# Kernel tuning notes

Hardware: AMD Instinct MI355X
Metric: run time of the kernel (lower is better)

## Reference

```python
import jax, jax.numpy as jnp
import numpy as np

B, C, H, W = 4, 256, 96, 96
FOUT = 32
HW = H * W
N = HW // 2  # inside/outside pixel counts (50/50 mask)


def setup_inputs() -> dict:
    key = jax.random.key(0)
    ks = jax.random.split(key, 6)
    f = jax.random.normal(ks[0], (B, C, H, W), dtype=jnp.float32)
    # deterministic alternating mask -> fixed N_in = N_out = HW/2 (jit-friendly)
    flat = (jnp.arange(HW) % 2).astype(jnp.float32)
    mask = jnp.broadcast_to(flat.reshape(1, 1, H, W), (B, 1, H, W))
    idx_in = jnp.nonzero(flat > 0.5, size=N)[0].astype(jnp.int32)   # mask == 1
    idx_out = jnp.nonzero(flat < 0.5, size=N)[0].astype(jnp.int32)  # mask == 0
    scale = 0.02
    Wq = jax.random.normal(ks[1], (FOUT, C), dtype=jnp.float32) * scale
    Wk = jax.random.normal(ks[2], (FOUT, C), dtype=jnp.float32) * scale
    Wv = jax.random.normal(ks[3], (C, C), dtype=jnp.float32) * scale
    bq = jnp.zeros((FOUT,), jnp.float32)
    bk = jnp.zeros((FOUT,), jnp.float32)
    bv = jnp.zeros((C,), jnp.float32)
    gamma = jax.random.uniform(ks[4], (1,), dtype=jnp.float32) + 0.25  # nonzero
    return {"f": f, "mask": mask, "idx_out": idx_out, "idx_in": idx_in,
            "Wq": Wq, "bq": bq, "Wk": Wk, "bk": bk, "Wv": Wv, "bv": bv,
            "gamma": gamma}


def reference(f, mask, idx_out, idx_in, Wq, bq, Wk, bk, Wv, bv, gamma):
    b, c, h, w = f.shape
    ff = f.reshape(b, c, h * w)              # (b, c, hw)
    f_out_pix = ff[:, :, idx_out]            # (b, c, Nout) gather outside pixels
    f_in_pix = ff[:, :, idx_in]              # (b, c, Nin)  gather inside pixels
    # 1x1 convs on gathered pixel sets == per-pixel linear projections
    q = jnp.einsum('oc,bcn->bon', Wq, f_out_pix) + bq[None, :, None]  # (b, fout, Nout)
    k = jnp.einsum('oc,bcn->bon', Wk, f_in_pix) + bk[None, :, None]   # (b, fout, Nin)
    v = jnp.einsum('dc,bcn->bdn', Wv, f_in_pix) + bv[None, :, None]   # (b, c, Nin)
    energy = jnp.einsum('boq,bok->bqk', q, k)       # (b, Nout, Nin)
    att = jax.nn.softmax(energy, axis=-1)
    r_v = jnp.einsum('bck,bqk->bcq', v, att)        # (b, c, Nout)
    ff2 = ff.at[:, :, idx_out].set(r_v)             # scatter write-back
    f_reshape = ff2.reshape(b, c, h, w)
    # NOTE: in torch, f_in aliases f's storage and is mutated by the scatter,
    # so f_in == f_reshape here. Reproduce that aliasing faithfully.
    f_out = f_reshape * (1.0 - mask) * gamma + f_reshape
    return (f_reshape, f_out)
```

## Files before the change

### kernel.cpp

```cpp
#include <hip/hip_runtime.h>
#include <math.h>

#define B_DIM    4
#define C_DIM    256
#define HW_DIM   9216
#define N_PIX    4608
#define FOUT_DIM 32
#define L2E      1.44269504f

typedef float  f32x4  __attribute__((ext_vector_type(4)));
typedef short  bf16x8 __attribute__((ext_vector_type(8)));

static __device__ __forceinline__ unsigned short f2bf(float x) {
    union { float f; unsigned int u; } v; v.f = x;
    unsigned int r = v.u + 0x7fffu + ((v.u >> 16) & 1u);
    return (unsigned short)(r >> 16);
}
static __device__ __forceinline__ float bf2f(unsigned short u) {
    union { unsigned int u; float f; } v; v.u = (unsigned int)u << 16; return v.f;
}

static __device__ __forceinline__ void gload_lds16(const unsigned short* g, unsigned short* l) {
    __builtin_amdgcn_global_load_lds(
        (const __attribute__((address_space(1))) void*)g,
        (__attribute__((address_space(3))) void*)l, 16, 0, 0);
}

__global__ __launch_bounds__(256) void gather_f(
    const float* __restrict__ f, const int* __restrict__ idx_out, const int* __restrict__ idx_in,
    unsigned short* __restrict__ Fo, unsigned short* __restrict__ Fi) {
    __shared__ float Fs[2][32][65];
    __shared__ int io[64], ii[64];
    const int t = threadIdx.x;
    const int n0 = blockIdx.x * 64, c0 = blockIdx.y * 32, b = blockIdx.z;
    if (t < 64) { io[t] = idx_out[n0 + t]; ii[t] = idx_in[n0 + t]; }
    __syncthreads();
    const float* fb = f + (size_t)b * C_DIM * HW_DIM;
    const int nn = t & 63, cg = t >> 6;
#pragma unroll
    for (int i = 0; i < 8; i++) {
        int c = cg * 8 + i;
        Fs[0][c][nn] = fb[(size_t)(c0 + c) * HW_DIM + io[nn]];
        Fs[1][c][nn] = fb[(size_t)(c0 + c) * HW_DIM + ii[nn]];
    }
    __syncthreads();
    {
        const int n = t >> 2, oc = (t & 3) * 8;
        size_t o = ((size_t)(b * N_PIX + n0 + n)) * C_DIM + c0 + oc;
        unsigned short tmp0[8], tmp1[8];
#pragma unroll
        for (int j = 0; j < 8; j++) {
            tmp0[j] = f2bf(Fs[0][oc + j][n]);
            tmp1[j] = f2bf(Fs[1][oc + j][n]);
        }
        *(uint4*)(Fo + o) = *(uint4*)tmp0;
        *(uint4*)(Fi + o) = *(uint4*)tmp1;
    }
}

#define FSP 40
__global__ __launch_bounds__(256) void prep(
    const unsigned short* __restrict__ Fo, const unsigned short* __restrict__ Fi,
    const float* __restrict__ Wq, const float* __restrict__ bq,
    const float* __restrict__ Wk, const float* __restrict__ bk,
    const float* __restrict__ Wv, const float* __restrict__ bv,
    unsigned short* __restrict__ Q, unsigned short* __restrict__ K,
    unsigned short* __restrict__ VT,
    const int* __restrict__ idx_out, const int* __restrict__ idx_in,
    int* __restrict__ inv) {
    __shared__ __align__(16) unsigned short SM[18688];
    const int bid = blockIdx.x, t = threadIdx.x;
    if (bid < 144) {
        unsigned short* Ws = SM;
        unsigned short* Fs = SM + 8448;
        const int n0 = (bid % 18) * 256, sel = (bid / 18) & 1, b = bid / 36;
        const unsigned short* FX = sel ? Fi : Fo;
        const float* W    = sel ? Wk : Wq;
        const float* bias = sel ? bk : bq;
        unsigned short* O = sel ? K : Q;
#pragma unroll
        for (int j = 0; j < 8; j++) {
            int fid = j * 256 + t, row = fid >> 6, f4 = fid & 63;
            float4 wv = *(const float4*)(W + (size_t)row * C_DIM + f4 * 4);
            uint2 pk;
            pk.x = f2bf(wv.x) | ((unsigned)f2bf(wv.y) << 16);
            pk.y = f2bf(wv.z) | ((unsigned)f2bf(wv.w) << 16);
            *(uint2*)(Ws + row * 264 + f4 * 4) = pk;
        }
        const int w = t >> 6, l = t & 63, lq = l & 15, lg = l >> 4;
        f32x4 acc[8];
#pragma unroll
        for (int i = 0; i < 8; i++) acc[i] = (f32x4){0.f, 0.f, 0.f, 0.f};
        for (int cs = 0; cs < 8; cs++) {
            __syncthreads();
#pragma unroll
            for (int j = 0; j < 4; j++) {
                int cid = j * 256 + t, row = cid >> 2, ch = cid & 3;
                *(uint4*)(Fs + row * FSP + ch * 8) =
                    *(const uint4*)(FX + ((size_t)(b * N_PIX + n0 + row)) * C_DIM + cs * 32 + ch * 8);
            }
            __syncthreads();
            bf16x8 bfr[2];
#pragma unroll
            for (int ob = 0; ob < 2; ob++)
                bfr[ob] = *(const bf16x8*)(Ws + (ob * 16 + lq) * 264 + cs * 32 + lg * 8);
#pragma unroll
            for (int ab = 0; ab < 4; ab++) {
                bf16x8 a = *(const bf16x8*)(Fs + (w * 64 + ab * 16 + lq) * FSP + lg * 8);
#pragma unroll
                for (int ob = 0; ob < 2; ob++)
                    acc[ab * 2 + ob] = __builtin_amdgcn_mfma_f32_16x16x32_bf16(a, bfr[ob], acc[ab * 2 + ob], 0, 0, 0);
            }
        }
#pragma unroll
        for (int ab = 0; ab < 4; ab++)
#pragma unroll
            for (int ob = 0; ob < 2; ob++)
#pragma unroll
                for (int r = 0; r < 4; r++) {
                    int n = n0 + w * 64 + ab * 16 + lg * 4 + r;
                    int o = ob * 16 + lq;
                    O[((size_t)(b * N_PIX + n)) * FOUT_DIM + o] = f2bf(acc[ab * 2 + ob][r] + bias[o]);
                }
    } else if (bid < 432) {
        unsigned short* Ws = SM;
        unsigned short* Fs = SM + 5120;
        const int vb = bid - 144;
        const int n0 = (vb % 36) * 128, d0 = ((vb / 36) & 1) * 128, b = vb / 72;
        const int w = t >> 6, wd = w & 1, wn = w >> 1, l = t & 63, lq = l & 15, lg = l >> 4;
        f32x4 acc[16];
#pragma unroll
        for (int i = 0; i < 16; i++) acc[i] = (f32x4){0.f, 0.f, 0.f, 0.f};
        for (int cs = 0; cs < 8; cs++) {
            __syncthreads();
#pragma unroll
            for (int j = 0; j < 4; j++) {
                int row = j * 32 + (t >> 3), f4 = t & 7;
                float4 wv = *(const float4*)(Wv + (size_t)(d0 + row) * C_DIM + cs * 32 + f4 * 4);
                uint2 pk;
                pk.x = f2bf(wv.x) | ((unsigned)f2bf(wv.y) << 16);
                pk.y = f2bf(wv.z) | ((unsigned)f2bf(wv.w) << 16);
                *(uint2*)(Ws + row * FSP + f4 * 4) = pk;
            }
#pragma unroll
            for (int j = 0; j < 2; j++) {
                int cid = j * 256 + t, row = cid >> 2, ch = cid & 3;
                *(uint4*)(Fs + row * FSP + ch * 8) =
                    *(const uint4*)(Fi + ((size_t)(b * N_PIX + n0 + row)) * C_DIM + cs * 32 + ch * 8);
            }
            __syncthreads();
            bf16x8 bfr[4];
#pragma unroll
            for (int nb = 0; nb < 4; nb++)
                bfr[nb] = *(const bf16x8*)(Fs + (wn * 64 + nb * 16 + lq) * FSP + lg * 8);
#pragma unroll
            for (int ab = 0; ab < 4; ab++) {
                bf16x8 a = *(const bf16x8*)(Ws + (wd * 64 + ab * 16 + lq) * FSP + lg * 8);
#pragma unroll
                for (int nb = 0; nb < 4; nb++)
                    acc[ab * 4 + nb] = __builtin_amdgcn_mfma_f32_16x16x32_bf16(a, bfr[nb], acc[ab * 4 + nb], 0, 0, 0);
            }
        }
#pragma unroll
        for (int ab = 0; ab < 4; ab++)
#pragma unroll
            for (int r = 0; r < 4; r++) {
                int d = d0 + wd * 64 + ab * 16 + lg * 4 + r;
                float bvv = bv[d];
#pragma unroll
                for (int nb = 0; nb < 4; nb++) {
                    int n = n0 + wn * 64 + nb * 16 + lq;
                    VT[((size_t)(b * C_DIM + d)) * N_PIX + n] = f2bf(acc[ab * 4 + nb][r] + bvv);
                }
            }
    } else {
        int i = (bid - 432) * 256 + t;
        if (i < N_PIX) {
            inv[idx_out[i]] = i;
            inv[idx_in[i]] = -1;
        }
    }
}

__global__ __launch_bounds__(256, 2) void flash_attn(
    const unsigned short* __restrict__ Q, const unsigned short* __restrict__ K,
    const unsigned short* __restrict__ VT,
    unsigned short* __restrict__ Rpart, float* __restrict__ lpart) {
    __shared__ __align__(16) unsigned short VB[256 * 64];
    __shared__ __align__(16) unsigned short PB[2][32 * 72];
    __shared__ float lred[2][2][2][16];
    const int t = threadIdx.x, w = t >> 6, l = t & 63, lq = l & 15, lg = l >> 4;
    const int qg = w & 1, dh = w >> 1;
    const int bid = blockIdx.x;
    const int bz = bid & 7, b = bz & 3, ks = bz >> 2;
    const int q0 = (bid >> 3) * 64 + qg * 32;
    const int d0 = dh * 128;
    const unsigned short* Qb = Q + (size_t)b * N_PIX * FOUT_DIM;
    const unsigned short* Kb = K + (size_t)b * N_PIX * FOUT_DIM;
    const unsigned short* Vb = VT + (size_t)b * C_DIM * N_PIX;
    unsigned short* Rp = Rpart + (size_t)ks * 4718592;
    float* lp = lpart + ks * (B_DIM * N_PIX);

    bf16x8 qfr[2];
    qfr[0] = *(const bf16x8*)(Qb + (size_t)(q0 + lq) * 32 + lg * 8);
    qfr[1] = *(const bf16x8*)(Qb + (size_t)(q0 + 16 + lq) * 32 + lg * 8);

    f32x4 acc[2][8];
#pragma unroll
    for (int qb = 0; qb < 2; qb++)
#pragma unroll
        for (int db = 0; db < 8; db++) acc[qb][db] = (f32x4){0.f, 0.f, 0.f, 0.f};
    float lsum[2] = {0.f, 0.f};

    int voff[8];
#pragma unroll
    for (int j = 0; j < 8; j++) {
        int row = (w * 8 + j) * 8 + (l >> 3);
        int ch  = (l & 7) ^ (row & 7);
        voff[j] = row * N_PIX + ch * 8;
    }
    const int kt0 = ks * 36;
    bf16x8 kpf[2];
    {
        int kg = kt0 * 64;
#pragma unroll
        for (int j = 0; j < 8; j++)
            gload_lds16(Vb + voff[j] + kg, VB + (w * 8 + j) * 512);
#pragma unroll
        for (int kb = 0; kb < 2; kb++)
            kpf[kb] = *(const bf16x8*)(Kb + (size_t)(kg + dh * 32 + kb * 16 + lq) * 32 + lg * 8);
    }

    const int swz = lq & 7;
#pragma unroll 1
    for (int it = 0; it < 36; it++) {
        {
            const f32x4 z4 = {0.f, 0.f, 0.f, 0.f};
#pragma unroll
            for (int qb = 0; qb < 2; qb++) {
                f32x4 s[2];
#pragma unroll
                for (int kb = 0; kb < 2; kb++)
                    s[kb] = __builtin_amdgcn_mfma_f32_16x16x32_bf16(kpf[kb], qfr[qb], z4, 0, 0, 0);
                float ps = 0.f;
#pragma unroll
                for (int kb = 0; kb < 2; kb++) {
                    float p0 = exp2f(s[kb][0] * L2E);
                    float p1 = exp2f(s[kb][1] * L2E);
                    float p2 = exp2f(s[kb][2] * L2E);
                    float p3 = exp2f(s[kb][3] * L2E);
                    ps += (p0 + p1) + (p2 + p3);
                    unsigned int u0 = (__float_as_uint(p0) + 0x8000u) >> 16;
                    unsigned int u1 = (__float_as_uint(p1) + 0x8000u) & 0xffff0000u;
                    unsigned int u2 = (__float_as_uint(p2) + 0x8000u) >> 16;
                    unsigned int u3 = (__float_as_uint(p3) + 0x8000u) & 0xffff0000u;
                    uint2 pk; pk.x = u0 | u1; pk.y = u2 | u3;
                    *(uint2*)(PB[qg] + (qb * 16 + lq) * 72 + dh * 32 + kb * 16 + lg * 4) = pk;
                }
                lsum[qb] += ps;
            }
        }
        __syncthreads();
        if (it + 1 < 36) {
            int kn = (kt0 + it + 1) * 64;
#pragma unroll
            for (int kb = 0; kb < 2; kb++)
                kpf[kb] = *(const bf16x8*)(Kb + (size_t)(kn + dh * 32 + kb * 16 + lq) * 32 + lg * 8);
        }
        bf16x8 af[2][2];
#pragma unroll
        for (int qb = 0; qb < 2; qb++) {
            af[qb][0] = *(const bf16x8*)(PB[qg] + (qb * 16 + lq) * 72 + lg * 8);
            af[qb][1] = *(const bf16x8*)(PB[qg] + (qb * 16 + lq) * 72 + 32 + lg * 8);
        }
#pragma unroll
        for (int db = 0; db < 8; db++) {
            int row = d0 + db * 16 + lq;
            bf16x8 b0 = *(const bf16x8*)(VB + row * 64 + (lg ^ swz) * 8);
            bf16x8 b1 = *(const bf16x8*)(VB + row * 64 + ((lg + 4) ^ swz) * 8);
#pragma unroll
            for (int qb = 0; qb < 2; qb++) {
                acc[qb][db] = __builtin_amdgcn_mfma_f32_16x16x32_bf16(af[qb][0], b0, acc[qb][db], 0, 0, 0);
                acc[qb][db] = __builtin_amdgcn_mfma_f32_16x16x32_bf16(af[qb][1], b1, acc[qb][db], 0, 0, 0);
            }
        }
        __syncthreads();
        if (it + 1 < 36) {
            int kn = (kt0 + it + 1) * 64;
#pragma unroll
            for (int j = 0; j < 8; j++)
                gload_lds16(Vb + voff[j] + kn, VB + (w * 8 + j) * 512);
        }
    }
#pragma unroll
    for (int qb = 0; qb < 2; qb++)
#pragma unroll
        for (int r = 0; r < 4; r++) {
            int q = q0 + qb * 16 + lg * 4 + r;
            unsigned short* rp = Rp + ((size_t)(b * N_PIX + q)) * C_DIM + d0;
#pragma unroll
            for (int db = 0; db < 8; db++)
                rp[db * 16 + lq] = f2bf(acc[qb][db][r]);
        }
#pragma unroll
    for (int qb = 0; qb < 2; qb++) {
        float v = lsum[qb];
        v += __shfl_xor(v, 16);
        v += __shfl_xor(v, 32);
        if (l < 16) lred[dh][qg][qb][l] = v;
    }
    __syncthreads();
    if (dh == 0 && l < 16) {
#pragma unroll
        for (int qb = 0; qb < 2; qb++)
            lp[b * N_PIX + q0 + qb * 16 + l] = lred[0][qg][qb][l] + lred[1][qg][qb][l];
    }
}

__global__ __launch_bounds__(256) void epilogue(
    const float* __restrict__ f, const float* __restrict__ mask,
    const unsigned short* __restrict__ R0, const unsigned short* __restrict__ R1,
    const float* __restrict__ l0, const float* __restrict__ l1,
    const int* __restrict__ inv, const float* __restrict__ gamma,
    float* __restrict__ out0, float* __restrict__ out1) {
    __shared__ __align__(16) unsigned short Rs0[32][264];
    __shared__ __align__(16) unsigned short Rs1[32][264];
    __shared__ int nns[32];
    __shared__ float lr[32];
    const int t = threadIdx.x, bid = blockIdx.x;
    const int b = bid / 288, p0 = (bid % 288) * 32;
    if (t < 32) {
        int n = inv[p0 + t];
        nns[t] = n;
        if (n >= 0) lr[t] = 1.0f / (l0[b * N_PIX + n] + l1[b * N_PIX + n]);
    }
    __syncthreads();
    {
        const int s = t >> 3, j = t & 7;
        int n = nns[s];
        if (n >= 0) {
            const unsigned short* r0 = R0 + ((size_t)(b * N_PIX + n)) * C_DIM;
            const unsigned short* r1 = R1 + ((size_t)(b * N_PIX + n)) * C_DIM;
#pragma unroll
            for (int k = 0; k < 4; k++) {
                int ch = j + k * 8;
                *(uint4*)(&Rs0[s][ch * 8]) = *(const uint4*)(r0 + ch * 8);
                *(uint4*)(&Rs1[s][ch * 8]) = *(const uint4*)(r1 + ch * 8);
            }
        }
    }
    __syncthreads();
    const float g = gamma[0];
    const int cg = t >> 3, po = (t & 7) * 4;
    float4 mv4 = *(const float4*)(mask + (size_t)b * HW_DIM + p0 + po);
    const float* mvp = (const float*)&mv4;
    int ns[4]; float lrv[4];
#pragma unroll
    for (int u = 0; u < 4; u++) {
        ns[u] = nns[po + u];
        lrv[u] = (ns[u] >= 0) ? lr[po + u] : 0.f;
    }
#pragma unroll
    for (int i = 0; i < 8; i++) {
        const int c = cg * 8 + i;
        const size_t e = ((size_t)(b * C_DIM + c)) * HW_DIM + p0 + po;
        float4 fv = *(const float4*)(f + e);
        const float* fvp = (const float*)&fv;
        float o0[4], o1[4];
#pragma unroll
        for (int u = 0; u < 4; u++) {
            float val;
            if (ns[u] >= 0) {
                int s = po + u;
                val = (bf2f(Rs0[s][c]) + bf2f(Rs1[s][c])) * lrv[u];
            } else {
                val = fvp[u];
            }
            o0[u] = val;
            o1[u] = val * (1.0f + g * (1.0f - mvp[u]));
        }
        *(float4*)(out0 + e) = make_float4(o0[0], o0[1], o0[2], o0[3]);
        *(float4*)(out1 + e) = make_float4(o1[0], o1[1], o1[2], o1[3]);
    }
}

extern "C" void kernel_launch(void* const* d_in, const int* in_sizes, int n_in,
                              void* d_out, int out_size, void* d_ws, size_t ws_size,
                              hipStream_t stream) {
    const float* f       = (const float*)d_in[0];
    const float* mask    = (const float*)d_in[1];
    const int*   idx_out = (const int*)d_in[2];
    const int*   idx_in  = (const int*)d_in[3];
    const float* Wq      = (const float*)d_in[4];
    const float* bq      = (const float*)d_in[5];
    const float* Wk      = (const float*)d_in[6];
    const float* bk      = (const float*)d_in[7];
    const float* Wv      = (const float*)d_in[8];
    const float* bv      = (const float*)d_in[9];
    const float* gamma   = (const float*)d_in[10];

    unsigned short* ws   = (unsigned short*)d_ws;
    unsigned short* Fo   = ws;
    unsigned short* Fi   = ws + 4718592;
    unsigned short* VTw  = ws + 9437184;
    unsigned short* Qw   = ws + 14155776;
    unsigned short* Kw   = ws + 14745600;
    float*          lptr = (float*)(ws + 15335424);
    int*            inv  = (int*)(lptr + 2 * B_DIM * N_PIX);
    unsigned short* Rpart = Fo;

    float* out0 = (float*)d_out;
    float* out1 = out0 + (size_t)B_DIM * C_DIM * HW_DIM;

    gather_f<<<dim3(72, 8, B_DIM), dim3(256), 0, stream>>>(f, idx_out, idx_in, Fo, Fi);
    prep<<<dim3(450), dim3(256), 0, stream>>>(Fo, Fi, Wq, bq, Wk, bk, Wv, bv,
                                              Qw, Kw, VTw, idx_out, idx_in, inv);
    flash_attn<<<dim3(576), dim3(256), 0, stream>>>(Qw, Kw, VTw, Rpart, lptr);
    epilogue<<<dim3(1152), dim3(256), 0, stream>>>(f, mask, Rpart, Rpart + 4718592,
                                                   lptr, lptr + B_DIM * N_PIX, inv, gamma, out0, out1);
}
```

Measured before the change: 234.8 us.

## Double-buffer prep GEMM tiles with async global-to-LDS loads and XOR swizzle

In the Q/K and V projection blocks of the prep kernel, the feature tiles are now loaded with global_load_lds directly into a double-buffered LDS region, and the next channel slice is prefetched while the current one is multiplied. The V path also double-buffers the bf16-converted Wv tile. Each loop iteration now uses one barrier instead of two. The feature tile layout drops its padding in favour of an XOR swizzle to avoid LDS bank conflicts. This costs more shared memory per block, which may reduce occupancy, and only affects the projection stage, not the attention.

```diff
diff --git a/kernel.cpp b/kernel.cpp
--- a/kernel.cpp
+++ b/kernel.cpp
@@ -68,11 +68,12 @@
     unsigned short* __restrict__ VT,
     const int* __restrict__ idx_out, const int* __restrict__ idx_in,
     int* __restrict__ inv) {
-    __shared__ __align__(16) unsigned short SM[18688];
+    __shared__ __align__(16) unsigned short SM[24832];
     const int bid = blockIdx.x, t = threadIdx.x;
+    const int lane = t & 63, wv = t >> 6;
     if (bid < 144) {
         unsigned short* Ws = SM;
-        unsigned short* Fs = SM + 8448;
+        unsigned short* Fb = SM + 8448;
         const int n0 = (bid % 18) * 256, sel = (bid / 18) & 1, b = bid / 36;
         const unsigned short* FX = sel ? Fi : Fo;
         const float* W    = sel ? Wk : Wq;
@@ -81,32 +82,44 @@
 #pragma unroll
         for (int j = 0; j < 8; j++) {
             int fid = j * 256 + t, row = fid >> 6, f4 = fid & 63;
-            float4 wv = *(const float4*)(W + (size_t)row * C_DIM + f4 * 4);
+            float4 wvv = *(const float4*)(W + (size_t)row * C_DIM + f4 * 4);
             uint2 pk;
-            pk.x = f2bf(wv.x) | ((unsigned)f2bf(wv.y) << 16);
-            pk.y = f2bf(wv.z) | ((unsigned)f2bf(wv.w) << 16);
+            pk.x = f2bf(wvv.x) | ((unsigned)f2bf(wvv.y) << 16);
+            pk.y = f2bf(wvv.z) | ((unsigned)f2bf(wvv.w) << 16);
             *(uint2*)(Ws + row * 264 + f4 * 4) = pk;
         }
-        const int w = t >> 6, l = t & 63, lq = l & 15, lg = l >> 4;
+        const int w = wv, l = lane, lq = l & 15, lg = l >> 4;
+        const int row_l = lane >> 2;
+        const int csrc = ((lane & 3) ^ (row_l & 3)) * 8;
         f32x4 acc[8];
 #pragma unroll
         for (int i = 0; i < 8; i++) acc[i] = (f32x4){0.f, 0.f, 0.f, 0.f};
+#pragma unroll
+        for (int j = 0; j < 4; j++) {
+            int g = j * 4 + wv, row = g * 16 + row_l;
+            gload_lds16(FX + (size_t)(b * N_PIX + n0 + row) * C_DIM + csrc,
+                        Fb + g * 512);
+        }
         for (int cs = 0; cs < 8; cs++) {
+            const int cur = cs & 1;
             __syncthreads();
-#pragma unroll
-            for (int j = 0; j < 4; j++) {
-                int cid = j * 256 + t, row = cid >> 2, ch = cid & 3;
-                *(uint4*)(Fs + row * FSP + ch * 8) =
-                    *(const uint4*)(FX + ((size_t)(b * N_PIX + n0 + row)) * C_DIM + cs * 32 + ch * 8);
-            }
-            __syncthreads();
+            if (cs + 1 < 8) {
+#pragma unroll
+                for (int j = 0; j < 4; j++) {
+                    int g = j * 4 + wv, row = g * 16 + row_l;
+                    gload_lds16(FX + (size_t)(b * N_PIX + n0 + row) * C_DIM + (cs + 1) * 32 + csrc,
+                                Fb + (cur ^ 1) * 8192 + g * 512);
+                }
+            }
+            const unsigned short* Fs = Fb + cur * 8192;
             bf16x8 bfr[2];
 #pragma unroll
             for (int ob = 0; ob < 2; ob++)
                 bfr[ob] = *(const bf16x8*)(Ws + (ob * 16 + lq) * 264 + cs * 32 + lg * 8);
 #pragma unroll
             for (int ab = 0; ab < 4; ab++) {
-                bf16x8 a = *(const bf16x8*)(Fs + (w * 64 + ab * 16 + lq) * FSP + lg * 8);
+                int row = w * 64 + ab * 16 + lq;
+                bf16x8 a = *(const bf16x8*)(Fs + row * 32 + ((lg ^ (lq & 3)) * 8));
 #pragma unroll
                 for (int ob = 0; ob < 2; ob++)
                     acc[ab * 2 + ob] = __builtin_amdgcn_mfma_f32_16x16x32_bf16(a, bfr[ob], acc[ab * 2 + ob], 0, 0, 0);
@@ -118,44 +131,67 @@
             for (int ob = 0; ob < 2; ob++)
 #pragma unroll
                 for (int r = 0; r < 4; r++) {
-                    int n = n0 + w * 64 + ab * 16 + lg * 4 + r;
-                    int o = ob * 16 + lq;
+                    int n = n0 + wv * 64 + ab * 16 + (lane >> 4) * 4 + r;
+                    int o = ob * 16 + (lane & 15);
                     O[((size_t)(b * N_PIX + n)) * FOUT_DIM + o] = f2bf(acc[ab * 2 + ob][r] + bias[o]);
                 }
     } else if (bid < 432) {
-        unsigned short* Ws = SM;
-        unsigned short* Fs = SM + 5120;
+        unsigned short* Wb = SM;
+        unsigned short* Fb = SM + 10240;
         const int vb = bid - 144;
         const int n0 = (vb % 36) * 128, d0 = ((vb / 36) & 1) * 128, b = vb / 72;
-        const int w = t >> 6, wd = w & 1, wn = w >> 1, l = t & 63, lq = l & 15, lg = l >> 4;
+        const int wd = wv & 1, wn = wv >> 1, l = lane, lq = l & 15, lg = l >> 4;
+        const int row_l = lane >> 2;
+        const int csrc = ((lane & 3) ^ (row_l & 3)) * 8;
         f32x4 acc[16];
 #pragma unroll
         for (int i = 0; i < 16; i++) acc[i] = (f32x4){0.f, 0.f, 0.f, 0.f};
+#pragma unroll
+        for (int j = 0; j < 4; j++) {
+            int row = j * 32 + (t >> 3), f4 = t & 7;
+            float4 wvv = *(const float4*)(Wv + (size_t)(d0 + row) * C_DIM + f4 * 4);
+            uint2 pk;
+            pk.x = f2bf(wvv.x) | ((unsigned)f2bf(wvv.y) << 16);
+            pk.y = f2bf(wvv.z) | ((unsigned)f2bf(wvv.w) << 16);
+            *(uint2*)(Wb + row * FSP + f4 * 4) = pk;
+        }
+#pragma unroll
+        for (int j = 0; j < 2; j++) {
+            int g = j * 4 + wv, row = g * 16 + row_l;
+            gload_lds16(Fi + (size_t)(b * N_PIX + n0 + row) * C_DIM + csrc,
+                        Fb + g * 512);
+        }
         for (int cs = 0; cs < 8; cs++) {
+            const int cur = cs & 1;
             __syncthreads();
-#pragma unroll
-            for (int j = 0; j < 4; j++) {
-                int row = j * 32 + (t >> 3), f4 = t & 7;
-                float4 wv = *(const float4*)(Wv + (size_t)(d0 + row) * C_DIM + cs * 32 + f4 * 4);
-                uint2 pk;
-                pk.x = f2bf(wv.x) | ((unsigned)f2bf(wv.y) << 16);
-                pk.y = f2bf(wv.z) | ((unsigned)f2bf(wv.w) << 16);
-                *(uint2*)(Ws + row * FSP + f4 * 4) = pk;
-            }
-#pragma unroll
-            for (int j = 0; j < 2; j++) {
-                int cid = j * 256 + t, row = cid >> 2, ch = cid & 3;
-                *(uint4*)(Fs + row * FSP + ch * 8) =
-                    *(const uint4*)(Fi + ((size_t)(b * N_PIX + n0 + row)) * C_DIM + cs * 32 + ch * 8);
-            }
-            __syncthreads();
+            if (cs + 1 < 8) {
+#pragma unroll
+                for (int j = 0; j < 2; j++) {
+                    int g = j * 4 + wv, row = g * 16 + row_l;
+                    gload_lds16(Fi + (size_t)(b * N_PIX + n0 + row) * C_DIM + (cs + 1) * 32 + csrc,
+                                Fb + (cur ^ 1) * 4096 + g * 512);
+                }
+#pragma unroll
+                for (int j = 0; j < 4; j++) {
+                    int row = j * 32 + (t >> 3), f4 = t & 7;
+                    float4 wvv = *(const float4*)(Wv + (size_t)(d0 + row) * C_DIM + (cs + 1) * 32 + f4 * 4);
+                    uint2 pk;
+                    pk.x = f2bf(wvv.x) | ((unsigned)f2bf(wvv.y) << 16);
+                    pk.y = f2bf(wvv.z) | ((unsigned)f2bf(wvv.w) << 16);
+                    *(uint2*)(Wb + (cur ^ 1) * 5120 + row * FSP + f4 * 4) = pk;
+                }
+            }
+            const unsigned short* Fs = Fb + cur * 4096;
+            const unsigned short* Wc = Wb + cur * 5120;
             bf16x8 bfr[4];
 #pragma unroll
-            for (int nb = 0; nb < 4; nb++)
-                bfr[nb] = *(const bf16x8*)(Fs + (wn * 64 + nb * 16 + lq) * FSP + lg * 8);
+            for (int nb = 0; nb < 4; nb++) {
+                int row = wn * 64 + nb * 16 + lq;
+                bfr[nb] = *(const bf16x8*)(Fs + row * 32 + ((lg ^ (lq & 3)) * 8));
+            }
 #pragma unroll
             for (int ab = 0; ab < 4; ab++) {
-                bf16x8 a = *(const bf16x8*)(Ws + (wd * 64 + ab * 16 + lq) * FSP + lg * 8);
+                bf16x8 a = *(const bf16x8*)(Wc + (wd * 64 + ab * 16 + lq) * FSP + lg * 8);
 #pragma unroll
                 for (int nb = 0; nb < 4; nb++)
                     acc[ab * 4 + nb] = __builtin_amdgcn_mfma_f32_16x16x32_bf16(a, bfr[nb], acc[ab * 4 + nb], 0, 0, 0);
```

Measured after the change: 231.0 us. About the same (-1.6%).
